# Performance work log

Hardware: AMD Instinct MI355X
Metric: run time of the kernel (lower is better)

Reference implementation:

```python
import jax, jax.numpy as jnp
import numpy as np

D_MODEL = 512
SEQ_LEN = 512
H = 8
D_K = D_MODEL // H  # 64
SCALE = 1.0 / float(np.sqrt(D_K))


def setup_inputs() -> dict:
    key = jax.random.key(0)
    ks = jax.random.split(key, 6)
    x_q = jax.random.normal(ks[0], (1, SEQ_LEN, D_MODEL), dtype=jnp.float32)
    x_k = jax.random.normal(ks[1], (1, SEQ_LEN, D_MODEL), dtype=jnp.float32)
    attention_mask = jnp.ones((1, SEQ_LEN), dtype=jnp.float32)
    # xavier-uniform-like init scale
    def xav(k, shape):
        lim = float(np.sqrt(6.0 / (shape[0] + shape[1])))
        return jax.random.uniform(k, shape, jnp.float32, -lim, lim)
    W_Q = xav(ks[2], (D_MODEL, D_K))
    W_K = xav(ks[3], (D_MODEL, D_K))
    W_V = xav(ks[4], (D_MODEL, D_K))
    W_O = xav(ks[5], (H * D_K, D_MODEL))
    return {"x_q": x_q, "x_k": x_k, "attention_mask": attention_mask,
            "W_Q": W_Q, "W_K": W_K, "W_V": W_V, "W_O": W_O}


def reference(x_q, x_k, attention_mask, W_Q, W_K, W_V, W_O):
    # Single-head attention (the original reuses the same W_Q/W_K/W_V for all 8 heads).
    Q = jnp.einsum('bsd,dk->bsk', x_q, W_Q)          # [1,S,64]
    K = jnp.einsum('bsd,dk->bsk', x_k, W_K)          # [1,S,64]
    V = jnp.einsum('bsd,dv->bsv', x_k, W_V)          # [1,S,64]
    # has_mask=False: causal_mask = ones(1,S,S) * attention_mask[:,None,:]
    mask = jnp.ones((1, SEQ_LEN, SEQ_LEN), dtype=x_q.dtype) * attention_mask[:, None, :]
    scores = SCALE * jnp.einsum('bsk,btk->bst', Q, K)  # [1,S,S]
    scores = jnp.where(mask == 0, -jnp.inf, scores)
    sm = jax.nn.softmax(scores, axis=-1)
    head = jnp.einsum('bst,btv->bsv', sm, V)         # [1,S,64]
    # All 8 heads are identical -> concatenation == tiling along feature dim.
    heads = jnp.tile(head, (1, 1, H))                 # [1,S,512]
    return heads @ W_O                                # [1,S,512]
```

## Files before the change

kernel.cpp:

```cpp
#include <hip/hip_runtime.h>
#include <math.h>

#define SEQ 512
#define DM  512
#define DK  64
#define NH  8
#define SCALE 0.125f

__global__ __launch_bounds__(512) void qkv_wor_kernel(
    const float* __restrict__ xq, const float* __restrict__ xk,
    const float* __restrict__ WQ, const float* __restrict__ WK,
    const float* __restrict__ WV, const float* __restrict__ WO,
    float* __restrict__ Q, float* __restrict__ K,
    float* __restrict__ V, float* __restrict__ Wor)
{
    const int b   = blockIdx.x;
    const int tid = threadIdx.x;

    if (b >= SEQ/2) {
        const int e = (b - SEQ/2) * 512 + tid;
        const int v = e >> 9, d = e & 511;
        float acc = 0.f;
        #pragma unroll
        for (int h = 0; h < NH; ++h) acc += WO[(h * DK + v) * DM + d];
        Wor[e] = acc;
        return;
    }

    const int r0 = 2 * b;
    __shared__ __align__(16) float xq_s[2][DM], xk_s[2][DM];
    __shared__ __align__(16) float part_s[3][8][2][DK];

    {
        if (tid < 256)
            reinterpret_cast<float4*>(xq_s)[tid] =
                reinterpret_cast<const float4*>(xq + r0 * DM)[tid];
        else
            reinterpret_cast<float4*>(xk_s)[tid - 256] =
                reinterpret_cast<const float4*>(xk + r0 * DM)[tid - 256];
    }
    __syncthreads();

    const int w    = tid >> 6;
    const int l    = tid & 63;
    const int dsub = l >> 4;
    const int kq   = (l & 15) * 4;

    float4 aq0{0,0,0,0}, aq1{0,0,0,0}, ak0{0,0,0,0},
           ak1{0,0,0,0}, av0{0,0,0,0}, av1{0,0,0,0};
    #pragma unroll
    for (int it = 0; it < 16; ++it) {
        const int d = w * 64 + it * 4 + dsub;
        const float4 wq = *reinterpret_cast<const float4*>(WQ + d * DK + kq);
        const float4 wk = *reinterpret_cast<const float4*>(WK + d * DK + kq);
        const float4 wv = *reinterpret_cast<const float4*>(WV + d * DK + kq);
        const float xq0 = xq_s[0][d], xq1 = xq_s[1][d];
        const float xk0 = xk_s[0][d], xk1 = xk_s[1][d];
        aq0.x += xq0*wq.x; aq0.y += xq0*wq.y; aq0.z += xq0*wq.z; aq0.w += xq0*wq.w;
        aq1.x += xq1*wq.x; aq1.y += xq1*wq.y; aq1.z += xq1*wq.z; aq1.w += xq1*wq.w;
        ak0.x += xk0*wk.x; ak0.y += xk0*wk.y; ak0.z += xk0*wk.z; ak0.w += xk0*wk.w;
        ak1.x += xk1*wk.x; ak1.y += xk1*wk.y; ak1.z += xk1*wk.z; ak1.w += xk1*wk.w;
        av0.x += xk0*wv.x; av0.y += xk0*wv.y; av0.z += xk0*wv.z; av0.w += xk0*wv.w;
        av1.x += xk1*wv.x; av1.y += xk1*wv.y; av1.z += xk1*wv.z; av1.w += xk1*wv.w;
    }
    #pragma unroll
    for (int off = 16; off < 64; off <<= 1) {
        aq0.x += __shfl_xor(aq0.x, off, 64); aq0.y += __shfl_xor(aq0.y, off, 64);
        aq0.z += __shfl_xor(aq0.z, off, 64); aq0.w += __shfl_xor(aq0.w, off, 64);
        aq1.x += __shfl_xor(aq1.x, off, 64); aq1.y += __shfl_xor(aq1.y, off, 64);
        aq1.z += __shfl_xor(aq1.z, off, 64); aq1.w += __shfl_xor(aq1.w, off, 64);
        ak0.x += __shfl_xor(ak0.x, off, 64); ak0.y += __shfl_xor(ak0.y, off, 64);
        ak0.z += __shfl_xor(ak0.z, off, 64); ak0.w += __shfl_xor(ak0.w, off, 64);
        ak1.x += __shfl_xor(ak1.x, off, 64); ak1.y += __shfl_xor(ak1.y, off, 64);
        ak1.z += __shfl_xor(ak1.z, off, 64); ak1.w += __shfl_xor(ak1.w, off, 64);
        av0.x += __shfl_xor(av0.x, off, 64); av0.y += __shfl_xor(av0.y, off, 64);
        av0.z += __shfl_xor(av0.z, off, 64); av0.w += __shfl_xor(av0.w, off, 64);
        av1.x += __shfl_xor(av1.x, off, 64); av1.y += __shfl_xor(av1.y, off, 64);
        av1.z += __shfl_xor(av1.z, off, 64); av1.w += __shfl_xor(av1.w, off, 64);
    }
    if (dsub == 0) {
        *reinterpret_cast<float4*>(&part_s[0][w][0][kq]) = aq0;
        *reinterpret_cast<float4*>(&part_s[0][w][1][kq]) = aq1;
        *reinterpret_cast<float4*>(&part_s[1][w][0][kq]) = ak0;
        *reinterpret_cast<float4*>(&part_s[1][w][1][kq]) = ak1;
        *reinterpret_cast<float4*>(&part_s[2][w][0][kq]) = av0;
        *reinterpret_cast<float4*>(&part_s[2][w][1][kq]) = av1;
    }
    __syncthreads();

    if (tid < 3 * 2 * DK) {
        const int m   = tid >> 7;
        const int rem = tid & 127;
        const int r   = rem >> 6;
        const int k   = rem & 63;
        float s = 0.f;
        #pragma unroll
        for (int p = 0; p < 8; ++p) s += part_s[m][p][r][k];
        float* dst = (m == 0) ? Q : (m == 1) ? K : V;
        dst[(r0 + r) * DK + k] = s;
    }
}

__global__ __launch_bounds__(512) void attn_out_kernel(
    const float* __restrict__ Q, const float* __restrict__ K,
    const float* __restrict__ V, const float* __restrict__ Wor,
    const float* __restrict__ amask, float* __restrict__ out)
{
    const int r0   = 2 * blockIdx.x;
    const int tid  = threadIdx.x;
    const int lane = tid & 63;
    const int w    = tid >> 6;
    const int dsub = lane >> 4;
    const int kq   = (lane & 15) * 4;

    __shared__ __align__(16) float q_s[2][DK];
    __shared__ float p_s[2][SEQ];
    __shared__ float red_s[2][8];
    __shared__ __align__(16) float hpart_s[2][8][DK];
    __shared__ __align__(16) float head_s[2][DK];
    __shared__ __align__(16) float4 epi_s[4][2][DM/4];

    if (tid < 2 * DK / 4)
        reinterpret_cast<float4*>(q_s)[tid] =
            reinterpret_cast<const float4*>(Q + r0 * DK)[tid];
    const float am = amask[tid];
    __syncthreads();

    float sc0 = 0.f, sc1 = 0.f;
    {
        const float4* k4 = reinterpret_cast<const float4*>(K + tid * DK);
        const float4* qa = reinterpret_cast<const float4*>(q_s[0]);
        const float4* qb = reinterpret_cast<const float4*>(q_s[1]);
        #pragma unroll
        for (int d = 0; d < DK / 4; ++d) {
            const float4 kv = k4[d], q0 = qa[d], q1 = qb[d];
            sc0 += q0.x*kv.x + q0.y*kv.y + q0.z*kv.z + q0.w*kv.w;
            sc1 += q1.x*kv.x + q1.y*kv.y + q1.z*kv.z + q1.w*kv.w;
        }
        sc0 *= SCALE; sc1 *= SCALE;
        if (am == 0.f) { sc0 = -INFINITY; sc1 = -INFINITY; }
    }

    float m0 = sc0, m1 = sc1;
    #pragma unroll
    for (int off = 32; off; off >>= 1) {
        m0 = fmaxf(m0, __shfl_xor(m0, off, 64));
        m1 = fmaxf(m1, __shfl_xor(m1, off, 64));
    }
    if (lane == 0) { red_s[0][w] = m0; red_s[1][w] = m1; }
    __syncthreads();
    float bmax0 = red_s[0][0], bmax1 = red_s[1][0];
    #pragma unroll
    for (int i = 1; i < 8; ++i) {
        bmax0 = fmaxf(bmax0, red_s[0][i]);
        bmax1 = fmaxf(bmax1, red_s[1][i]);
    }
    __syncthreads();

    const float p0 = __expf(sc0 - bmax0);
    const float p1 = __expf(sc1 - bmax1);
    p_s[0][tid] = p0;  p_s[1][tid] = p1;
    float s0 = p0, s1 = p1;
    #pragma unroll
    for (int off = 32; off; off >>= 1) {
        s0 += __shfl_xor(s0, off, 64);
        s1 += __shfl_xor(s1, off, 64);
    }
    if (lane == 0) { red_s[0][w] = s0; red_s[1][w] = s1; }
    __syncthreads();
    float bs0 = 0.f, bs1 = 0.f;
    #pragma unroll
    for (int i = 0; i < 8; ++i) { bs0 += red_s[0][i]; bs1 += red_s[1][i]; }
    const float inv0 = 1.f / bs0, inv1 = 1.f / bs1;

    float4 h0{0,0,0,0}, h1{0,0,0,0};
    #pragma unroll
    for (int it = 0; it < 16; ++it) {
        const int t = w * 64 + it * 4 + dsub;
        const float4 v4 = *reinterpret_cast<const float4*>(V + t * DK + kq);
        const float pa = p_s[0][t], pb = p_s[1][t];
        h0.x += pa*v4.x; h0.y += pa*v4.y; h0.z += pa*v4.z; h0.w += pa*v4.w;
        h1.x += pb*v4.x; h1.y += pb*v4.y; h1.z += pb*v4.z; h1.w += pb*v4.w;
    }
    #pragma unroll
    for (int off = 16; off < 64; off <<= 1) {
        h0.x += __shfl_xor(h0.x, off, 64); h0.y += __shfl_xor(h0.y, off, 64);
        h0.z += __shfl_xor(h0.z, off, 64); h0.w += __shfl_xor(h0.w, off, 64);
        h1.x += __shfl_xor(h1.x, off, 64); h1.y += __shfl_xor(h1.y, off, 64);
        h1.z += __shfl_xor(h1.z, off, 64); h1.w += __shfl_xor(h1.w, off, 64);
    }
    if (dsub == 0) {
        *reinterpret_cast<float4*>(&hpart_s[0][w][kq]) = h0;
        *reinterpret_cast<float4*>(&hpart_s[1][w][kq]) = h1;
    }
    __syncthreads();
    if (tid < 2 * DK) {
        const int r = tid >> 6, k = tid & 63;
        float hs = 0.f;
        #pragma unroll
        for (int p = 0; p < 8; ++p) hs += hpart_s[r][p][k];
        head_s[r][k] = hs * (r == 0 ? inv0 : inv1);
    }
    __syncthreads();

    {
        const int dq = tid & 127;
        const int vc = tid >> 7;
        float4 o0{0,0,0,0}, o1{0,0,0,0};
        #pragma unroll
        for (int j = 0; j < 16; ++j) {
            const int v = vc * 16 + j;
            const float4 wv = reinterpret_cast<const float4*>(Wor)[v * (DM/4) + dq];
            const float ha = head_s[0][v], hb = head_s[1][v];
            o0.x += ha*wv.x; o0.y += ha*wv.y; o0.z += ha*wv.z; o0.w += ha*wv.w;
            o1.x += hb*wv.x; o1.y += hb*wv.y; o1.z += hb*wv.z; o1.w += hb*wv.w;
        }
        epi_s[vc][0][dq] = o0;
        epi_s[vc][1][dq] = o1;
    }
    __syncthreads();
    if (tid < 256) {
        const int r = tid >> 7, dq = tid & 127;
        const float4 a = epi_s[0][r][dq], b2 = epi_s[1][r][dq];
        const float4 c = epi_s[2][r][dq], d2 = epi_s[3][r][dq];
        float4 s;
        s.x = a.x + b2.x + c.x + d2.x;
        s.y = a.y + b2.y + c.y + d2.y;
        s.z = a.z + b2.z + c.z + d2.z;
        s.w = a.w + b2.w + c.w + d2.w;
        reinterpret_cast<float4*>(out)[(r0 + r) * (DM/4) + dq] = s;
    }
}

extern "C" void kernel_launch(void* const* d_in, const int* in_sizes, int n_in,
                              void* d_out, int out_size, void* d_ws, size_t ws_size,
                              hipStream_t stream) {
    const float* xq    = (const float*)d_in[0];
    const float* xk    = (const float*)d_in[1];
    const float* amask = (const float*)d_in[2];
    const float* WQ    = (const float*)d_in[3];
    const float* WK    = (const float*)d_in[4];
    const float* WV    = (const float*)d_in[5];
    const float* WO    = (const float*)d_in[6];
    float* out = (float*)d_out;

    float* ws  = (float*)d_ws;
    float* Q   = ws;
    float* K   = ws + SEQ * DK;
    float* V   = ws + 2 * SEQ * DK;
    float* Wor = ws + 3 * SEQ * DK;

    qkv_wor_kernel<<<SEQ/2 + DK, 512, 0, stream>>>(xq, xk, WQ, WK, WV, WO, Q, K, V, Wor);
    attn_out_kernel<<<SEQ/2, 512, 0, stream>>>(Q, K, V, Wor, amask, out);
}
```

Measured before the change: 22.09 us.

## Drop softmax max pass, fold Wor reduction into idle QKV threads

The Wor head-sum moves into the 128 otherwise idle threads of each QKV block, so the 64 extra blocks are no longer launched. The attention kernel drops the max-subtraction reduction and its barriers. It preloads K rows into registers, passes probabilities between lanes by shuffle instead of through shared memory, and accumulates the softmax denominator alongside the PV product. The output projection now uses 256 threads, each looping over all 64 values, in place of the 4-way split plus shared-memory reduction. Skipping the max subtraction risks exp overflow for large scores, and the epilogue uses fewer threads.

```diff
diff --git a/kernel.cpp b/kernel.cpp
--- a/kernel.cpp
+++ b/kernel.cpp
@@ -16,18 +16,8 @@
 {
     const int b   = blockIdx.x;
     const int tid = threadIdx.x;
-
-    if (b >= SEQ/2) {
-        const int e = (b - SEQ/2) * 512 + tid;
-        const int v = e >> 9, d = e & 511;
-        float acc = 0.f;
-        #pragma unroll
-        for (int h = 0; h < NH; ++h) acc += WO[(h * DK + v) * DM + d];
-        Wor[e] = acc;
-        return;
-    }
-
-    const int r0 = 2 * b;
+    const int r0  = 2 * b;
+
     __shared__ __align__(16) float xq_s[2][DM], xk_s[2][DM];
     __shared__ __align__(16) float part_s[3][8][2][DK];
 
@@ -98,6 +88,13 @@
         for (int p = 0; p < 8; ++p) s += part_s[m][p][r][k];
         float* dst = (m == 0) ? Q : (m == 1) ? K : V;
         dst[(r0 + r) * DK + k] = s;
+    } else {
+        const int e = b * 128 + (tid - 384);
+        const int v = e >> 9, d = e & 511;
+        float acc = 0.f;
+        #pragma unroll
+        for (int h = 0; h < NH; ++h) acc += WO[(h * DK + v) * DM + d];
+        Wor[e] = acc;
     }
 }
 
@@ -114,12 +111,16 @@
     const int kq   = (lane & 15) * 4;
 
     __shared__ __align__(16) float q_s[2][DK];
-    __shared__ float p_s[2][SEQ];
-    __shared__ float red_s[2][8];
     __shared__ __align__(16) float hpart_s[2][8][DK];
+    __shared__ float psum_s[2][8];
     __shared__ __align__(16) float head_s[2][DK];
-    __shared__ __align__(16) float4 epi_s[4][2][DM/4];
-
+
+    float4 kreg[16];
+    {
+        const float4* k4 = reinterpret_cast<const float4*>(K + tid * DK);
+        #pragma unroll
+        for (int d = 0; d < 16; ++d) kreg[d] = k4[d];
+    }
     if (tid < 2 * DK / 4)
         reinterpret_cast<float4*>(q_s)[tid] =
             reinterpret_cast<const float4*>(Q + r0 * DK)[tid];
@@ -128,59 +129,30 @@
 
     float sc0 = 0.f, sc1 = 0.f;
     {
-        const float4* k4 = reinterpret_cast<const float4*>(K + tid * DK);
         const float4* qa = reinterpret_cast<const float4*>(q_s[0]);
         const float4* qb = reinterpret_cast<const float4*>(q_s[1]);
         #pragma unroll
         for (int d = 0; d < DK / 4; ++d) {
-            const float4 kv = k4[d], q0 = qa[d], q1 = qb[d];
+            const float4 kv = kreg[d], q0 = qa[d], q1 = qb[d];
             sc0 += q0.x*kv.x + q0.y*kv.y + q0.z*kv.z + q0.w*kv.w;
             sc1 += q1.x*kv.x + q1.y*kv.y + q1.z*kv.z + q1.w*kv.w;
         }
-        sc0 *= SCALE; sc1 *= SCALE;
-        if (am == 0.f) { sc0 = -INFINITY; sc1 = -INFINITY; }
-    }
-
-    float m0 = sc0, m1 = sc1;
-    #pragma unroll
-    for (int off = 32; off; off >>= 1) {
-        m0 = fmaxf(m0, __shfl_xor(m0, off, 64));
-        m1 = fmaxf(m1, __shfl_xor(m1, off, 64));
-    }
-    if (lane == 0) { red_s[0][w] = m0; red_s[1][w] = m1; }
-    __syncthreads();
-    float bmax0 = red_s[0][0], bmax1 = red_s[1][0];
-    #pragma unroll
-    for (int i = 1; i < 8; ++i) {
-        bmax0 = fmaxf(bmax0, red_s[0][i]);
-        bmax1 = fmaxf(bmax1, red_s[1][i]);
-    }
-    __syncthreads();
-
-    const float p0 = __expf(sc0 - bmax0);
-    const float p1 = __expf(sc1 - bmax1);
-    p_s[0][tid] = p0;  p_s[1][tid] = p1;
-    float s0 = p0, s1 = p1;
-    #pragma unroll
-    for (int off = 32; off; off >>= 1) {
-        s0 += __shfl_xor(s0, off, 64);
-        s1 += __shfl_xor(s1, off, 64);
-    }
-    if (lane == 0) { red_s[0][w] = s0; red_s[1][w] = s1; }
-    __syncthreads();
-    float bs0 = 0.f, bs1 = 0.f;
-    #pragma unroll
-    for (int i = 0; i < 8; ++i) { bs0 += red_s[0][i]; bs1 += red_s[1][i]; }
-    const float inv0 = 1.f / bs0, inv1 = 1.f / bs1;
+    }
+    const float p0 = (am == 0.f) ? 0.f : __expf(sc0 * SCALE);
+    const float p1 = (am == 0.f) ? 0.f : __expf(sc1 * SCALE);
 
     float4 h0{0,0,0,0}, h1{0,0,0,0};
+    float ps0 = 0.f, ps1 = 0.f;
     #pragma unroll
     for (int it = 0; it < 16; ++it) {
-        const int t = w * 64 + it * 4 + dsub;
+        const int src = it * 4 + dsub;
+        const float pa = __shfl(p0, src, 64);
+        const float pb = __shfl(p1, src, 64);
+        const int t = w * 64 + src;
         const float4 v4 = *reinterpret_cast<const float4*>(V + t * DK + kq);
-        const float pa = p_s[0][t], pb = p_s[1][t];
         h0.x += pa*v4.x; h0.y += pa*v4.y; h0.z += pa*v4.z; h0.w += pa*v4.w;
         h1.x += pb*v4.x; h1.y += pb*v4.y; h1.z += pb*v4.z; h1.w += pb*v4.w;
+        ps0 += pa; ps1 += pb;
     }
     #pragma unroll
     for (int off = 16; off < 64; off <<= 1) {
@@ -188,47 +160,37 @@
         h0.z += __shfl_xor(h0.z, off, 64); h0.w += __shfl_xor(h0.w, off, 64);
         h1.x += __shfl_xor(h1.x, off, 64); h1.y += __shfl_xor(h1.y, off, 64);
         h1.z += __shfl_xor(h1.z, off, 64); h1.w += __shfl_xor(h1.w, off, 64);
+        ps0  += __shfl_xor(ps0, off, 64);
+        ps1  += __shfl_xor(ps1, off, 64);
     }
     if (dsub == 0) {
         *reinterpret_cast<float4*>(&hpart_s[0][w][kq]) = h0;
         *reinterpret_cast<float4*>(&hpart_s[1][w][kq]) = h1;
-    }
-    __syncthreads();
+        if (lane == 0) { psum_s[0][w] = ps0; psum_s[1][w] = ps1; }
+    }
+    __syncthreads();
+
     if (tid < 2 * DK) {
         const int r = tid >> 6, k = tid & 63;
-        float hs = 0.f;
-        #pragma unroll
-        for (int p = 0; p < 8; ++p) hs += hpart_s[r][p][k];
-        head_s[r][k] = hs * (r == 0 ? inv0 : inv1);
-    }
-    __syncthreads();
-
-    {
+        float hs = 0.f, den = 0.f;
+        #pragma unroll
+        for (int p = 0; p < 8; ++p) { hs += hpart_s[r][p][k]; den += psum_s[r][p]; }
+        head_s[r][k] = hs / den;
+    }
+    __syncthreads();
+
+    if (tid < 256) {
+        const int r  = tid >> 7;
         const int dq = tid & 127;
-        const int vc = tid >> 7;
-        float4 o0{0,0,0,0}, o1{0,0,0,0};
-        #pragma unroll
-        for (int j = 0; j < 16; ++j) {
-            const int v = vc * 16 + j;
-            const float4 wv = reinterpret_cast<const float4*>(Wor)[v * (DM/4) + dq];
-            const float ha = head_s[0][v], hb = head_s[1][v];
-            o0.x += ha*wv.x; o0.y += ha*wv.y; o0.z += ha*wv.z; o0.w += ha*wv.w;
-            o1.x += hb*wv.x; o1.y += hb*wv.y; o1.z += hb*wv.z; o1.w += hb*wv.w;
+        const float4* wor4 = reinterpret_cast<const float4*>(Wor);
+        float4 o{0,0,0,0};
+        #pragma unroll 8
+        for (int v = 0; v < DK; ++v) {
+            const float4 wv = wor4[v * (DM/4) + dq];
+            const float h = head_s[r][v];
+            o.x += h*wv.x; o.y += h*wv.y; o.z += h*wv.z; o.w += h*wv.w;
         }
-        epi_s[vc][0][dq] = o0;
-        epi_s[vc][1][dq] = o1;
-    }
-    __syncthreads();
-    if (tid < 256) {
-        const int r = tid >> 7, dq = tid & 127;
-        const float4 a = epi_s[0][r][dq], b2 = epi_s[1][r][dq];
-        const float4 c = epi_s[2][r][dq], d2 = epi_s[3][r][dq];
-        float4 s;
-        s.x = a.x + b2.x + c.x + d2.x;
-        s.y = a.y + b2.y + c.y + d2.y;
-        s.z = a.z + b2.z + c.z + d2.z;
-        s.w = a.w + b2.w + c.w + d2.w;
-        reinterpret_cast<float4*>(out)[(r0 + r) * (DM/4) + dq] = s;
+        reinterpret_cast<float4*>(out)[(r0 + r) * (DM/4) + dq] = o;
     }
 }
 
@@ -250,6 +212,6 @@
     float* V   = ws + 2 * SEQ * DK;
     float* Wor = ws + 3 * SEQ * DK;
 
-    qkv_wor_kernel<<<SEQ/2 + DK, 512, 0, stream>>>(xq, xk, WQ, WK, WV, WO, Q, K, V, Wor);
+    qkv_wor_kernel<<<SEQ/2, 512, 0, stream>>>(xq, xk, WQ, WK, WV, WO, Q, K, V, Wor);
     attn_out_kernel<<<SEQ/2, 512, 0, stream>>>(Q, K, V, Wor, amask, out);
 }
```

New measurement: 22.56 us. 2.1% more time.
